# Optimization experiments

Hardware: AMD Instinct MI355X
Metric: run time of the kernel (lower is better)

The kernel has to match this reference:

```python
import jax, jax.numpy as jnp
import numpy as np

B, S, D = 4, 2048, 1024
N_NEURONS, K = 512, 8
N_BASIS, R = 32, 512
N_HEADS = 8
D_HEAD = R // N_HEADS


def setup_inputs() -> dict:
    key = jax.random.key(0)
    ks = jax.random.split(key, 8)
    x = jax.random.normal(ks[0], (B, S, D), dtype=jnp.float32)
    W_router = jax.random.normal(ks[1], (N_NEURONS, D), dtype=jnp.float32) / np.sqrt(D)
    recipe_Q = jax.random.normal(ks[2], (N_NEURONS, N_BASIS), dtype=jnp.float32)
    recipe_K = jax.random.normal(ks[3], (N_NEURONS, N_BASIS), dtype=jnp.float32)
    recipe_V = jax.random.normal(ks[4], (N_NEURONS, N_BASIS), dtype=jnp.float32)
    # orthonormal basis: QR of random [D, R] per basis slot (buffer, not trained)
    raw = jax.random.normal(ks[5], (N_BASIS, D, R), dtype=jnp.float32)
    basis = jax.vmap(lambda m: jnp.linalg.qr(m)[0])(raw)  # [N_BASIS, D, R]
    W_o = jax.random.normal(ks[6], (D, R), dtype=jnp.float32) / np.sqrt(R)
    mask = jnp.tril(jnp.ones((S, S), dtype=jnp.int32))[None, None]  # [1,1,S,S] causal
    mask = jnp.broadcast_to(mask, (B, 1, S, S))
    return {"x": x, "W_router": W_router, "recipe_Q": recipe_Q, "recipe_K": recipe_K,
            "recipe_V": recipe_V, "basis": basis, "W_o": W_o, "mask": mask}


def reference(x, W_router, recipe_Q, recipe_K, recipe_V, basis, W_o, mask):
    # routing: pick top-k neurons per token
    scores = jnp.einsum('bsd,nd->bsn', x, W_router)            # [B,S,N_NEURONS]
    topk_scores, topk_idx = jax.lax.top_k(scores, K)            # [B,S,K]
    weights = jax.nn.softmax(topk_scores, axis=-1)              # [B,S,K]

    def token_recipe(recipe):
        g = recipe[topk_idx]                                    # [B,S,K,N_BASIS]
        r = jnp.einsum('bskn,bsk->bsn', g, weights)             # [B,S,N_BASIS]
        return jax.nn.softmax(r, axis=-1)

    tQ = token_recipe(recipe_Q)
    tK = token_recipe(recipe_K)
    tV = token_recipe(recipe_V)

    # shared basis projection of x, reused for Q/K/V (same math as
    # W = einsum('bsn,ndr->bsdr'); Q = einsum('bsd,bsdr->bsr'))
    P = jnp.einsum('bsd,ndr->bsnr', x, basis)                   # [B,S,N_BASIS,R]
    Q = jnp.einsum('bsnr,bsn->bsr', P, tQ)
    Kt = jnp.einsum('bsnr,bsn->bsr', P, tK)
    V = jnp.einsum('bsnr,bsn->bsr', P, tV)

    def heads(t):
        return t.reshape(B, S, N_HEADS, D_HEAD).transpose(0, 2, 1, 3)  # [B,H,S,dh]

    Qh, Kh, Vh = heads(Q), heads(Kt), heads(V)
    attn = jnp.einsum('bhqd,bhkd->bhqk', Qh, Kh) / np.sqrt(D_HEAD)
    attn = jnp.where(mask == 0, jnp.float32(-1e30), attn)
    attn = jax.nn.softmax(attn, axis=-1)                        # dropout p: eval/no-op
    out = jnp.einsum('bhqk,bhkd->bhqd', attn, Vh)
    out = out.transpose(0, 2, 1, 3).reshape(B, S, R)
    attn_out = jnp.einsum('bsr,dr->bsd', out, W_o)
    return attn_out, topk_idx, weights
```

## Files before the change

### kernel.cpp

```cpp
#include <hip/hip_runtime.h>
#include <math.h>
#include <stdint.h>


typedef __attribute__((ext_vector_type(4))) float f32x4;
typedef __attribute__((ext_vector_type(8))) short s16x8;
typedef __attribute__((ext_vector_type(4))) short s16x4;
typedef __attribute__((ext_vector_type(2))) long longx2;

#define DEV __device__ __forceinline__

DEV short f2bf(float f){
  union { float f; unsigned u; } c; c.f = f;
  unsigned u = c.u;
  unsigned r = (u + 0x7fffu + ((u >> 16) & 1u)) >> 16;
  return (short)r;
}
DEV float bf2f(short s){
  union { unsigned u; float f; } c; c.u = ((unsigned)(unsigned short)s) << 16;
  return c.f;
}
DEV unsigned char f2e4m3(float f){
  union { float f; unsigned u; } c; c.f = f;
  unsigned u = c.u;
  unsigned sign = (u >> 24) & 0x80u;
  unsigned a = u & 0x7fffffffu;
  if (a >= 0x43e00000u) return (unsigned char)(sign | 0x7Eu);
  if (a < 0x3c800000u){
    union { unsigned u; float f; } d; d.u = a;
    int q = (int)(d.f * 512.0f + 0.5f);
    return (unsigned char)(sign | (unsigned)q);
  }
  unsigned m = a & 0x7fffffu;
  unsigned e = (a >> 23) - 120u;
  unsigned keep = m >> 20;
  unsigned rest = m & 0xFFFFFu;
  if (rest > 0x80000u || (rest == 0x80000u && (keep & 1u))){
    keep++;
    if (keep == 8u){ keep = 0; e++; }
  }
  if (e >= 16u || (e == 15u && keep == 7u)) return (unsigned char)(sign | 0x7Eu);
  return (unsigned char)(sign | (e << 3) | keep);
}

typedef __attribute__((address_space(3))) void lds_vt;
typedef const __attribute__((address_space(1))) void g_vt;
DEV void gload16(const void* g, void* lds){
  __builtin_amdgcn_global_load_lds((g_vt*)g, (lds_vt*)lds, 16, 0, 0);
}

DEV int kperm_byte(int d){
  int cg = (d >> 3) & 7;
  return (d & ~63) + (cg < 4 ? (cg << 4) : (((cg - 4) << 4) + 8));
}

__global__ void k_conv_bf16(const float* __restrict__ in, short* __restrict__ out, int n4){
  int i = blockIdx.x*256 + threadIdx.x;
  if (i >= n4) return;
  float4 v = ((const float4*)in)[i];
  s16x4 o; o[0]=f2bf(v.x); o[1]=f2bf(v.y); o[2]=f2bf(v.z); o[3]=f2bf(v.w);
  ((s16x4*)out)[i] = o;
}

__global__ void k_conv_xf8(const float* __restrict__ in, char* __restrict__ out){
  int t = blockIdx.x*256 + threadIdx.x;
  int row = t >> 7, cch = t & 127;
  int d = cch << 3;
  int pbyte = kperm_byte(d);
  const float4* s = (const float4*)(in + (size_t)row*1024 + d);
  float4 a = s[0], b = s[1];
  float vals[8] = {a.x,a.y,a.z,a.w,b.x,b.y,b.z,b.w};
  unsigned long long v = 0;
  #pragma unroll
  for (int e=0;e<8;e++) v |= ((unsigned long long)f2e4m3(vals[e])) << (8*e);
  *(unsigned long long*)(out + (size_t)row*1024 + pbyte) = v;
}

__global__ __launch_bounds__(256) void k_conv_basis8(const float* __restrict__ basis, char* __restrict__ B2f){
  __shared__ float tile[64][65];
  int tid = threadIdx.x;
  int r0 = blockIdx.x<<6, d0 = blockIdx.y<<6, n = blockIdx.z;
  const float* src = basis + ((size_t)n*1024 + d0)*512 + r0;
  for (int i = tid; i < 4096; i += 256){ int dd = i>>6, rr = i&63; tile[dd][rr] = src[(size_t)dd*512 + rr]; }
  __syncthreads();
  for (int t = tid; t < 512; t += 256){
    int rr = t >> 3, c8 = t & 7;
    int d = d0 + (c8 << 3);
    int pbyte = kperm_byte(d);
    unsigned long long v = 0;
    #pragma unroll
    for (int e=0;e<8;e++) v |= ((unsigned long long)f2e4m3(tile[(c8<<3)+e][rr])) << (8*e);
    *(unsigned long long*)(B2f + ((size_t)(r0+rr)*32 + n)*1024 + pbyte) = v;
  }
}

__global__ __launch_bounds__(256) void k_gemm_c32(
    const short* __restrict__ A, const short* __restrict__ Bt, int Kd, int Mblk,
    float* __restrict__ C, int ldc)
{
  __shared__ char smem[32768];
  short* Asm = (short*)smem;
  short* Bsm = (short*)(smem + 16384);
  int tid = threadIdx.x, lane = tid & 63, w = tid >> 6;
  int wr = w >> 1, wc = w & 1;
  int nwg = gridDim.x, bid = blockIdx.x;
  int sid = (bid & 7) * (nwg >> 3) + (bid >> 3);
  int row0 = (sid % Mblk) << 7;
  int col0 = (sid / Mblk) << 7;
  f32x4 acc[4][4];
  #pragma unroll
  for (int m=0;m<4;m++)
    #pragma unroll
    for (int nf=0;nf<4;nf++)
      #pragma unroll
      for (int e=0;e<4;e++) acc[m][nf][e] = 0.f;
  int lr8 = lane >> 3;
  int lk_sw = (((lane & 7) ^ (lane >> 3)) << 3);
  for (int k0 = 0; k0 < Kd; k0 += 64){
    #pragma unroll
    for (int i=0;i<4;i++){
      int chunk = (w<<2) + i;
      int r = (chunk<<3) + lr8;
      gload16(A  + (size_t)(row0 + r)*Kd + k0 + lk_sw, smem + chunk*1024);
      gload16(Bt + (size_t)(col0 + r)*Kd + k0 + lk_sw, smem + 16384 + chunk*1024);
    }
    __syncthreads();
    #pragma unroll
    for (int kk=0; kk<2; kk++){
      int csw = (kk*32 + ((lane>>4)<<3)) ^ ((lane & 7) << 3);
      s16x8 af[4], bfr[4];
      #pragma unroll
      for (int m=0;m<4;m++)
        af[m] = *(const s16x8*)(Asm + ((wr*64 + m*16 + (lane&15))*64 + csw));
      #pragma unroll
      for (int nf=0;nf<4;nf++)
        bfr[nf] = *(const s16x8*)(Bsm + ((wc*64 + nf*16 + (lane&15))*64 + csw));
      #pragma unroll
      for (int m=0;m<4;m++)
        #pragma unroll
        for (int nf=0;nf<4;nf++)
          acc[m][nf] = __builtin_amdgcn_mfma_f32_16x16x32_bf16(af[m], bfr[nf], acc[m][nf], 0, 0, 0);
    }
    __syncthreads();
  }
  #pragma unroll
  for (int m=0;m<4;m++)
    #pragma unroll
    for (int nf=0;nf<4;nf++)
      #pragma unroll
      for (int e=0;e<4;e++){
        int tok = wr*64 + m*16 + ((lane>>4)<<2) + e;
        int col = wc*64 + nf*16 + (lane&15);
        C[(size_t)(row0+tok)*ldc + col0 + col] = acc[m][nf][e];
      }
}

#define STAGE8(G, tileRow0, half, tkt) do{ \
  int _t = (tkt) < 7 ? (tkt) : 7; \
  char* _d = smem + ((G)==Xf8 ? 65536 : 0) + ((_t&1)*32768) + ((half)*16384) + (wid*2048); \
  const char* _s = (G) + (size_t)((tileRow0) + (half)*128 + wid*16 + (lane>>3))*1024 + (_t<<7) + (((lane&7)^(lane>>3))<<4); \
  gload16(_s, _d); \
  gload16(_s + 8192, _d + 1024); \
}while(0)

#define LD_AF8(dst, base) \
  _Pragma("unroll") \
  for (int i=0;i<4;i++){ \
    const char* _p = (base) + (wm*64 + i*16 + l15)*128; \
    _Pragma("unroll") \
    for (int pp=0;pp<2;pp++) \
      dst[i][pp] = *(const longx2*)(_p + ((((pp<<2)+g16) ^ l7)<<4)); \
  }

#define LD_BF8(dst, base) \
  _Pragma("unroll") \
  for (int n=0;n<2;n++){ \
    const char* _p = (base) + (wn*32 + n*16 + l15)*128; \
    _Pragma("unroll") \
    for (int pp=0;pp<2;pp++) \
      dst[n][pp] = *(const longx2*)(_p + ((((pp<<2)+g16) ^ l7)<<4)); \
  }

#define VMC(N) asm volatile("s_waitcnt vmcnt(" #N ")" ::: "memory")
#define PBAR() do{ __builtin_amdgcn_sched_barrier(0); __builtin_amdgcn_s_barrier(); }while(0)

#define MFMA_Q8(Q, AF, BF) do{ \
  __builtin_amdgcn_s_setprio(1); \
  _Pragma("unroll") \
  for (int pp=0;pp<2;pp++) \
    _Pragma("unroll") \
    for (int h=0;h<2;h++) \
      _Pragma("unroll") \
      for (int i=0;i<4;i++) \
        _Pragma("unroll") \
        for (int n=0;n<2;n++) \
          acc[Q][i][n] = __builtin_amdgcn_mfma_f32_16x16x32_fp8_fp8(AF[i][pp][h], BF[n][pp][h], acc[Q][i][n], 0,0,0); \
  __builtin_amdgcn_s_setprio(0); \
}while(0)

__global__ __launch_bounds__(512, 2) void k_pgemm8(
    const char* __restrict__ B2f, const char* __restrict__ Xf8,
    const float* __restrict__ tQp, const float* __restrict__ tKp, const float* __restrict__ tVp,
    short* __restrict__ Qb, short* __restrict__ Kb, short* __restrict__ Vt)
{
  extern __shared__ char smem[];
  int tid = threadIdx.x, lane = tid & 63, wid = tid >> 6;
  int wm = wid >> 2, wn = wid & 3;
  int l15 = lane & 15, l7 = lane & 7, g16 = lane >> 4;
  int bid = blockIdx.x;
  int xcd = bid & 7, lid = bid >> 3;
  int t_tile = (xcd << 2) + (lid & 3);
  int c_tile = lid >> 2;
  int row0 = c_tile << 8;
  int col0 = t_tile << 8;

  f32x4 acc[4][4][2];
  #pragma unroll
  for (int q=0;q<4;q++)
    #pragma unroll
    for (int m=0;m<4;m++)
      #pragma unroll
      for (int n=0;n<2;n++)
        #pragma unroll
        for (int e=0;e<4;e++) acc[q][m][n][e] = 0.f;
  longx2 af[4][2], bf0[2][2], bf1[2][2];

  STAGE8(B2f, row0, 0, 0);
  STAGE8(Xf8, col0, 0, 0);
  STAGE8(Xf8, col0, 1, 0);
  STAGE8(B2f, row0, 1, 0);
  VMC(4);
  PBAR();

  for (int kt = 0; kt < 8; ++kt){
    const char* Ac = smem + (kt&1)*32768;
    const char* Bc = smem + 65536 + (kt&1)*32768;
    LD_AF8(af,  Ac);
    LD_BF8(bf0, Bc);
    STAGE8(B2f, row0, 0, kt+1);
    VMC(4);
    PBAR();
    MFMA_Q8(0, af, bf0);
    LD_BF8(bf1, Bc + 16384);
    STAGE8(Xf8, col0, 0, kt+1);
    VMC(4);
    PBAR();
    MFMA_Q8(1, af, bf1);
    LD_AF8(af, Ac + 16384);
    STAGE8(Xf8, col0, 1, kt+1);
    PBAR();
    MFMA_Q8(2, af, bf0);
    STAGE8(B2f, row0, 1, kt+1);
    VMC(4);
    PBAR();
    MFMA_Q8(3, af, bf1);
  }

  VMC(0);
  __syncthreads();
  short* t16 = (short*)smem;
  for (int i = tid; i < 8192; i += 512){
    int tk = i >> 5, n = i & 31;
    t16[tk*36 + n]            = f2bf(tQp[(size_t)col0*32 + i]);
    t16[9216 + tk*36 + n]     = f2bf(tKp[(size_t)col0*32 + i]);
    t16[18432 + tk*36 + n]    = f2bf(tVp[(size_t)col0*32 + i]);
  }
  __syncthreads();
  int g4 = g16 << 2;
  #pragma unroll
  for (int rec=0; rec<3; rec++){
    const short* tb = t16 + rec*9216;
    #pragma unroll
    for (int q=0;q<4;q++){
      int rb = (row0 >> 5) + (q>>1)*4 + wm*2;
      #pragma unroll
      for (int n=0;n<2;n++){
        int tok = (q&1)*128 + wn*32 + n*16 + l15;
        s16x4 tlo = *(const s16x4*)(tb + tok*36 + g4);
        s16x4 thi = *(const s16x4*)(tb + tok*36 + 16 + g4);
        #pragma unroll
        for (int mp=0;mp<2;mp++){
          float p = 0.f;
          #pragma unroll
          for (int e=0;e<4;e++) p += acc[q][2*mp][n][e]   * bf2f(tlo[e]);
          #pragma unroll
          for (int e=0;e<4;e++) p += acc[q][2*mp+1][n][e] * bf2f(thi[e]);
          p += __shfl_xor(p, 16);
          p += __shfl_xor(p, 32);
          if (g16 == rec){
            int gtok = col0 + tok;
            int r = rb + mp;
            if (rec == 0)      Qb[(size_t)gtok*512 + r] = f2bf(p);
            else if (rec == 1) Kb[(size_t)gtok*512 + r] = f2bf(p);
            else Vt[(((size_t)(gtok>>11)*8 + (r>>6))*64 + (r&63))*2048 + (gtok&2047)] = f2bf(p);
          }
        }
      }
    }
  }
}

__global__ __launch_bounds__(64) void k_router(const float* __restrict__ scores,
    const float* __restrict__ X, const float* __restrict__ W,
    const float* __restrict__ rQ, const float* __restrict__ rK, const float* __restrict__ rV,
    float* __restrict__ tQ, float* __restrict__ tK, float* __restrict__ tV,
    float* __restrict__ oidx, float* __restrict__ ow){
  int token = blockIdx.x; int lane = threadIdx.x;
  const float* srow = scores + (size_t)token*512;
  float v[8];
  #pragma unroll
  for (int j=0;j<8;j++) v[j] = srow[lane + 64*j];
  int myidx = 0x7fffffff;
  #pragma unroll
  for (int k=0;k<16;k++){
    float bm = -INFINITY; int bi = 0x7fffffff;
    #pragma unroll
    for (int j=0;j<8;j++){ if (v[j] > bm) { bm = v[j]; bi = lane + 64*j; } }
    #pragma unroll
    for (int off=32; off>=1; off>>=1){
      float om = __shfl_xor(bm, off); int oi = __shfl_xor(bi, off);
      if (om > bm || (om == bm && oi < bi)) { bm = om; bi = oi; }
    }
    if (lane == k) myidx = bi;
    #pragma unroll
    for (int j=0;j<8;j++) if (lane + 64*j == bi) v[j] = -INFINITY;
  }
  float xr[16];
  {
    const float4* x4 = (const float4*)(X + (size_t)token*1024 + lane*16);
    #pragma unroll
    for (int q=0;q<4;q++){ float4 t = x4[q]; xr[q*4]=t.x; xr[q*4+1]=t.y; xr[q*4+2]=t.z; xr[q*4+3]=t.w; }
  }
  double myref = -1e300;
  #pragma unroll
  for (int c=0;c<16;c++){
    int nid = __shfl(myidx, c);
    const float4* w4 = (const float4*)(W + (size_t)nid*1024 + lane*16);
    double acc = 0.0;
    #pragma unroll
    for (int q=0;q<4;q++){
      float4 t = w4[q];
      acc += (double)xr[q*4]   * (double)t.x;
      acc += (double)xr[q*4+1] * (double)t.y;
      acc += (double)xr[q*4+2] * (double)t.z;
      acc += (double)xr[q*4+3] * (double)t.w;
    }
    #pragma unroll
    for (int off=32; off>=1; off>>=1) acc += __shfl_xor(acc, off);
    if (lane == c) myref = acc;
  }
  double mv = myref; int mi = myidx;
  double topv[8]; int topi[8];
  #pragma unroll
  for (int k=0;k<8;k++){
    double bm = mv; int bi = mi;
    #pragma unroll
    for (int off=32; off>=1; off>>=1){
      double om = __shfl_xor(bm, off); int oi = __shfl_xor(bi, off);
      if (om > bm || (om == bm && oi < bi)) { bm = om; bi = oi; }
    }
    topv[k]=bm; topi[k]=bi;
    if (mi == bi) mv = -1e300;
  }
  double mx = topv[0]; double s = 0.0; double wd[8];
  #pragma unroll
  for (int k=0;k<8;k++){ wd[k] = exp(topv[k]-mx); s += wd[k]; }
  float w[8];
  #pragma unroll
  for (int k=0;k<8;k++) w[k] = (float)(wd[k]/s);
  if (lane == 0){
    #pragma unroll
    for (int k=0;k<8;k++){ oidx[(size_t)token*8+k] = (float)topi[k]; ow[(size_t)token*8+k] = w[k]; }
  }
  int n = lane & 31;
  float aq=0.f, ak=0.f, av=0.f;
  #pragma unroll
  for (int k=0;k<8;k++){
    size_t off = (size_t)topi[k]*32 + n;
    aq += w[k]*rQ[off]; ak += w[k]*rK[off]; av += w[k]*rV[off];
  }
  float mq = aq, mk2 = ak, mvv = av;
  #pragma unroll
  for (int off=16; off>=1; off>>=1){
    mq  = fmaxf(mq,  __shfl_xor(mq, off));
    mk2 = fmaxf(mk2, __shfl_xor(mk2,off));
    mvv = fmaxf(mvv, __shfl_xor(mvv,off));
  }
  float eq = expf(aq-mq), ek = expf(ak-mk2), ev = expf(av-mvv);
  float sq = eq, sk = ek, sv = ev;
  #pragma unroll
  for (int off=16; off>=1; off>>=1){
    sq += __shfl_xor(sq,off); sk += __shfl_xor(sk,off); sv += __shfl_xor(sv,off);
  }
  if (lane < 32){
    tQ[(size_t)token*32+n] = eq/sq;
    tK[(size_t)token*32+n] = ek/sk;
    tV[(size_t)token*32+n] = ev/sv;
  }
}

__global__ __launch_bounds__(256) void k_attn(const short* __restrict__ Qb, const short* __restrict__ Kb,
                                              const short* __restrict__ Vt, short* __restrict__ Ob)
{
  __shared__ char smem[40960];
  int tid = threadIdx.x, lane = tid & 63, wid = tid >> 6;
  int l15 = lane & 15, l7 = lane & 7, g16 = lane >> 4;
  int bid = blockIdx.x;
  int xcd = bid & 7, lid = bid >> 3;
  int work = xcd*128 + lid;
  int bx = 31 - (work & 31);
  int bh = work >> 5; int h = bh & 7, b = bh >> 3;
  size_t tokbase = (size_t)b*2048;
  int q0 = bx << 6;
  int nt = bx + 1;
  const float SC = 0.125f * 1.44269504f;

#define ATTN_STAGE(kt_) do{ \
  int _c = (kt_) & 1; \
  _Pragma("unroll") \
  for (int _i=0;_i<2;_i++){ \
    int _row = _i*32 + (wid<<3) + (lane>>3); \
    gload16(Kb + (tokbase + (((kt_)<<6) + _row))*512 + (h<<6) + ((l7 ^ (_row&7))<<3), \
            smem + (_c<<13) + _i*4096 + (wid<<10) + lane*16); \
    gload16(Vt + (size_t)((bh<<6) + _row)*2048 + ((kt_)<<6) + ((l7 ^ (_row&7))<<3), \
            smem + 16384 + (_c<<13) + _i*4096 + (wid<<10) + lane*16); \
  } \
}while(0)

  s16x8 qf[2];
  {
    const short* qp = Qb + (tokbase + q0 + wid*16 + l15)*512 + (h<<6);
    qf[0] = *(const s16x8*)(qp + g16*8);
    qf[1] = *(const s16x8*)(qp + 32 + g16*8);
  }
  int q_abs = q0 + wid*16 + l15;
  f32x4 o[4];
  float m_log = -INFINITY, l_sum = 0.f;
  #pragma unroll
  for (int i=0;i<4;i++)
    #pragma unroll
    for (int e=0;e<4;e++) o[i][e]=0.f;

  ATTN_STAGE(0);
  __syncthreads();

  for (int kt = 0; kt < nt; ++kt){
    if (kt + 1 < nt) ATTN_STAGE(kt+1);
    int cur = kt & 1;
    const char* Kc = smem + (cur<<13);
    const char* Vc = smem + 16384 + (cur<<13);
    char* Pb = smem + 32768 + (wid<<11);
    f32x4 S[4];
    #pragma unroll
    for (int s16=0;s16<4;s16++){
      #pragma unroll
      for (int e=0;e<4;e++) S[s16][e] = 0.f;
      const char* kr = Kc + (s16*16 + l15)*128;
      s16x8 kf0 = *(const s16x8*)(kr + (((g16  ) ^ l7)<<4));
      s16x8 kf1 = *(const s16x8*)(kr + (((4+g16) ^ l7)<<4));
      S[s16] = __builtin_amdgcn_mfma_f32_16x16x32_bf16(kf0, qf[0], S[s16], 0,0,0);
      S[s16] = __builtin_amdgcn_mfma_f32_16x16x32_bf16(kf1, qf[1], S[s16], 0,0,0);
    }
    bool diag = (kt == nt-1);
    float sm[16];
    #pragma unroll
    for (int s16=0;s16<4;s16++)
      #pragma unroll
      for (int e=0;e<4;e++){
        float sv = S[s16][e] * SC;
        if (diag){
          int kv_abs = (kt<<6) + s16*16 + (g16<<2) + e;
          if (kv_abs > q_abs) sv = -1e30f;
        }
        sm[s16*4+e] = sv;
      }
    float pmax = sm[0];
    #pragma unroll
    for (int j=1;j<16;j++) pmax = fmaxf(pmax, sm[j]);
    pmax = fmaxf(pmax, __shfl_xor(pmax, 16));
    pmax = fmaxf(pmax, __shfl_xor(pmax, 32));
    float mnew = fmaxf(m_log, pmax);
    float alpha = exp2f(m_log - mnew);
    m_log = mnew;
    float p[16], ps = 0.f;
    #pragma unroll
    for (int j=0;j<16;j++){ p[j] = exp2f(sm[j] - mnew); ps += p[j]; }
    ps += __shfl_xor(ps, 16);
    ps += __shfl_xor(ps, 32);
    l_sum = l_sum*alpha + ps;
    #pragma unroll
    for (int e=0;e<4;e++){
      float al = __shfl(alpha, (g16<<2)+e);
      #pragma unroll
      for (int df=0;df<4;df++) o[df][e] *= al;
    }
    #pragma unroll
    for (int s16=0;s16<4;s16++){
      s16x4 pk;
      #pragma unroll
      for (int e=0;e<4;e++) pk[e] = f2bf(p[s16*4+e]);
      *(s16x4*)(Pb + l15*128 + (((s16<<5) + (g16<<3)) ^ (l7<<4))) = pk;
    }
    s16x8 pf0 = *(const s16x8*)(Pb + l15*128 + (((g16  ) ^ l7)<<4));
    s16x8 pf1 = *(const s16x8*)(Pb + l15*128 + (((4+g16) ^ l7)<<4));
    #pragma unroll
    for (int df=0;df<4;df++){
      const char* vr = Vc + (df*16 + l15)*128;
      s16x8 vf0 = *(const s16x8*)(vr + (((g16  ) ^ l7)<<4));
      s16x8 vf1 = *(const s16x8*)(vr + (((4+g16) ^ l7)<<4));
      o[df] = __builtin_amdgcn_mfma_f32_16x16x32_bf16(pf0, vf0, o[df], 0,0,0);
      o[df] = __builtin_amdgcn_mfma_f32_16x16x32_bf16(pf1, vf1, o[df], 0,0,0);
    }
    __syncthreads();
  }
  #pragma unroll
  for (int e=0;e<4;e++){
    float ln = __shfl(l_sum, (g16<<2)+e);
    float inv = 1.0f / ln;
    #pragma unroll
    for (int df=0;df<4;df++){
      int q = q0 + wid*16 + (g16<<2) + e;
      int d = df*16 + l15;
      Ob[(tokbase + q)*512 + (h<<6) + d] = f2bf(o[df][e] * inv);
    }
  }
#undef ATTN_STAGE
}

extern "C" void kernel_launch(void* const* d_in, const int* in_sizes, int n_in,
                              void* d_out, int out_size, void* d_ws, size_t ws_size,
                              hipStream_t stream)
{
  const float* x     = (const float*)d_in[0];
  const float* Wrt   = (const float*)d_in[1];
  const float* rQ    = (const float*)d_in[2];
  const float* rK    = (const float*)d_in[3];
  const float* rV    = (const float*)d_in[4];
  const float* basis = (const float*)d_in[5];
  const float* Wo    = (const float*)d_in[6];
  float* out = (float*)d_out;
  char* ws = (char*)d_ws;
  char*  B2f  = (char*)(ws + 0);
  char*  Xf8  = (char*)(ws + 16777216);
  short* Xb   = (short*)(ws + 25165824);
  float* SC   = (float*)(ws + 41943040);
  float* tQ   = (float*)(ws + 58720256);
  float* tK   = (float*)(ws + 59768832);
  float* tV   = (float*)(ws + 60817408);
  short* Qb   = (short*)(ws + 61865984);
  short* Kb   = (short*)(ws + 70254592);
  short* Vt   = (short*)(ws + 78643200);
  short* Ob   = (short*)(ws + 87031808);
  short* Wob  = (short*)(ws + 95420416);
  short* Wrtb = (short*)(ws + 96468992);
  float* oidx = out + 8388608;
  float* oww  = out + 8454144;

  hipFuncSetAttribute((const void*)k_pgemm8, hipFuncAttributeMaxDynamicSharedMemorySize, 131072);

  k_conv_bf16<<<8192, 256, 0, stream>>>(x, Xb, 2097152);
  k_conv_xf8<<<4096, 256, 0, stream>>>(x, Xf8);
  k_conv_bf16<<<512, 256, 0, stream>>>(Wo, Wob, 131072);
  k_conv_bf16<<<512, 256, 0, stream>>>(Wrt, Wrtb, 131072);
  k_conv_basis8<<<dim3(8,16,32), 256, 0, stream>>>(basis, B2f);
  k_gemm_c32<<<256, 256, 0, stream>>>(Xb, Wrtb, 1024, 64, SC, 512);
  k_router<<<8192, 64, 0, stream>>>(SC, x, Wrt, rQ, rK, rV, tQ, tK, tV, oidx, oww);
  k_pgemm8<<<2048, 512, 131072, stream>>>(B2f, Xf8, tQ, tK, tV, Qb, Kb, Vt);
  k_attn<<<1024, 256, 0, stream>>>(Qb, Kb, Vt, Ob);
  k_gemm_c32<<<512, 256, 0, stream>>>(Ob, Wob, 512, 64, out, 1024);
}
```

Measured before the change: 460.7 us.

## Switch projection GEMM to 16x16x128 scaled FP8 MFMA and fuse x conversions

Replaces the 16x16x32 fp8 MFMA with the gfx950 scaled 16x16x128 f8f6f4 MFMA, using unit scales (0x7f). Because each lane now reads 32 contiguous bytes of K, the K-permutation applied when writing the fp8 x and basis tensors is removed. It also merges the bf16 and fp8 conversions of x into a single kernel that reads x once. The intent is fewer MFMA instructions, higher MFMA throughput, and one less pass over x. The risk is that the new register and LDS read pattern must match the operand layout this instruction expects.

```diff
diff --git a/kernel.cpp b/kernel.cpp
--- a/kernel.cpp
+++ b/kernel.cpp
@@ -6,7 +6,8 @@
 typedef __attribute__((ext_vector_type(4))) float f32x4;
 typedef __attribute__((ext_vector_type(8))) short s16x8;
 typedef __attribute__((ext_vector_type(4))) short s16x4;
-typedef __attribute__((ext_vector_type(2))) long longx2;
+typedef __attribute__((ext_vector_type(4))) int i32x4;
+typedef __attribute__((ext_vector_type(8))) int i32x8;
 
 #define DEV __device__ __forceinline__
 
@@ -49,11 +50,6 @@
   __builtin_amdgcn_global_load_lds((g_vt*)g, (lds_vt*)lds, 16, 0, 0);
 }
 
-DEV int kperm_byte(int d){
-  int cg = (d >> 3) & 7;
-  return (d & ~63) + (cg < 4 ? (cg << 4) : (((cg - 4) << 4) + 8));
-}
-
 __global__ void k_conv_bf16(const float* __restrict__ in, short* __restrict__ out, int n4){
   int i = blockIdx.x*256 + threadIdx.x;
   if (i >= n4) return;
@@ -62,18 +58,20 @@
   ((s16x4*)out)[i] = o;
 }
 
-__global__ void k_conv_xf8(const float* __restrict__ in, char* __restrict__ out){
+__global__ void k_conv_x(const float* __restrict__ in, short* __restrict__ Xb, char* __restrict__ Xf8){
   int t = blockIdx.x*256 + threadIdx.x;
-  int row = t >> 7, cch = t & 127;
-  int d = cch << 3;
-  int pbyte = kperm_byte(d);
-  const float4* s = (const float4*)(in + (size_t)row*1024 + d);
+  const float4* s = (const float4*)(in + (size_t)t*8);
   float4 a = s[0], b = s[1];
   float vals[8] = {a.x,a.y,a.z,a.w,b.x,b.y,b.z,b.w};
+  s16x8 ob;
   unsigned long long v = 0;
   #pragma unroll
-  for (int e=0;e<8;e++) v |= ((unsigned long long)f2e4m3(vals[e])) << (8*e);
-  *(unsigned long long*)(out + (size_t)row*1024 + pbyte) = v;
+  for (int e=0;e<8;e++){
+    ob[e] = f2bf(vals[e]);
+    v |= ((unsigned long long)f2e4m3(vals[e])) << (8*e);
+  }
+  *(s16x8*)(Xb + (size_t)t*8) = ob;
+  *(unsigned long long*)(Xf8 + (size_t)t*8) = v;
 }
 
 __global__ __launch_bounds__(256) void k_conv_basis8(const float* __restrict__ basis, char* __restrict__ B2f){
@@ -85,12 +83,10 @@
   __syncthreads();
   for (int t = tid; t < 512; t += 256){
     int rr = t >> 3, c8 = t & 7;
-    int d = d0 + (c8 << 3);
-    int pbyte = kperm_byte(d);
     unsigned long long v = 0;
     #pragma unroll
     for (int e=0;e<8;e++) v |= ((unsigned long long)f2e4m3(tile[(c8<<3)+e][rr])) << (8*e);
-    *(unsigned long long*)(B2f + ((size_t)(r0+rr)*32 + n)*1024 + pbyte) = v;
+    *(unsigned long long*)(B2f + ((size_t)(r0+rr)*32 + n)*1024 + d0 + (c8<<3)) = v;
   }
 }
 
@@ -167,18 +163,20 @@
   _Pragma("unroll") \
   for (int i=0;i<4;i++){ \
     const char* _p = (base) + (wm*64 + i*16 + l15)*128; \
-    _Pragma("unroll") \
-    for (int pp=0;pp<2;pp++) \
-      dst[i][pp] = *(const longx2*)(_p + ((((pp<<2)+g16) ^ l7)<<4)); \
+    i32x4 _t0 = *(const i32x4*)(_p + ((((g16<<1)  ) ^ l7)<<4)); \
+    i32x4 _t1 = *(const i32x4*)(_p + ((((g16<<1)+1) ^ l7)<<4)); \
+    dst[i][0]=_t0[0]; dst[i][1]=_t0[1]; dst[i][2]=_t0[2]; dst[i][3]=_t0[3]; \
+    dst[i][4]=_t1[0]; dst[i][5]=_t1[1]; dst[i][6]=_t1[2]; dst[i][7]=_t1[3]; \
   }
 
 #define LD_BF8(dst, base) \
   _Pragma("unroll") \
   for (int n=0;n<2;n++){ \
     const char* _p = (base) + (wn*32 + n*16 + l15)*128; \
-    _Pragma("unroll") \
-    for (int pp=0;pp<2;pp++) \
-      dst[n][pp] = *(const longx2*)(_p + ((((pp<<2)+g16) ^ l7)<<4)); \
+    i32x4 _t0 = *(const i32x4*)(_p + ((((g16<<1)  ) ^ l7)<<4)); \
+    i32x4 _t1 = *(const i32x4*)(_p + ((((g16<<1)+1) ^ l7)<<4)); \
+    dst[n][0]=_t0[0]; dst[n][1]=_t0[1]; dst[n][2]=_t0[2]; dst[n][3]=_t0[3]; \
+    dst[n][4]=_t1[0]; dst[n][5]=_t1[1]; dst[n][6]=_t1[2]; dst[n][7]=_t1[3]; \
   }
 
 #define VMC(N) asm volatile("s_waitcnt vmcnt(" #N ")" ::: "memory")
@@ -187,14 +185,11 @@
 #define MFMA_Q8(Q, AF, BF) do{ \
   __builtin_amdgcn_s_setprio(1); \
   _Pragma("unroll") \
-  for (int pp=0;pp<2;pp++) \
+  for (int i=0;i<4;i++) \
     _Pragma("unroll") \
-    for (int h=0;h<2;h++) \
-      _Pragma("unroll") \
-      for (int i=0;i<4;i++) \
-        _Pragma("unroll") \
-        for (int n=0;n<2;n++) \
-          acc[Q][i][n] = __builtin_amdgcn_mfma_f32_16x16x32_fp8_fp8(AF[i][pp][h], BF[n][pp][h], acc[Q][i][n], 0,0,0); \
+    for (int n=0;n<2;n++) \
+      acc[Q][i][n] = __builtin_amdgcn_mfma_scale_f32_16x16x128_f8f6f4( \
+          AF[i], BF[n], acc[Q][i][n], 0, 0, 0, 0x7f7f7f7f, 0, 0x7f7f7f7f); \
   __builtin_amdgcn_s_setprio(0); \
 }while(0)
 
@@ -223,7 +218,7 @@
       for (int n=0;n<2;n++)
         #pragma unroll
         for (int e=0;e<4;e++) acc[q][m][n][e] = 0.f;
-  longx2 af[4][2], bf0[2][2], bf1[2][2];
+  i32x8 af[4], bf0[2], bf1[2];
 
   STAGE8(B2f, row0, 0, 0);
   STAGE8(Xf8, col0, 0, 0);
@@ -558,8 +553,7 @@
 
   hipFuncSetAttribute((const void*)k_pgemm8, hipFuncAttributeMaxDynamicSharedMemorySize, 131072);
 
-  k_conv_bf16<<<8192, 256, 0, stream>>>(x, Xb, 2097152);
-  k_conv_xf8<<<4096, 256, 0, stream>>>(x, Xf8);
+  k_conv_x<<<4096, 256, 0, stream>>>(x, Xb, Xf8);
   k_conv_bf16<<<512, 256, 0, stream>>>(Wo, Wob, 131072);
   k_conv_bf16<<<512, 256, 0, stream>>>(Wrt, Wrtb, 131072);
   k_conv_basis8<<<dim3(8,16,32), 256, 0, stream>>>(basis, B2f);
```

New measurement: 410.7 us. 1.12x faster.
